# Kernel optimization log

Hardware: AMD Instinct MI355X
Metric: run time of the kernel (lower is better)

Reference implementation:

```python
import jax, jax.numpy as jnp
import numpy as np

N_EMBED = 768
NUM_HEADS = 12
HEAD_SIZE = N_EMBED // NUM_HEADS
EPS = 1e-6


def layer_norm(x, gamma, beta):
    # torch .var() is unbiased (ddof=1)
    mean = x.mean(-1, keepdims=True)
    var = jnp.var(x, axis=-1, keepdims=True, ddof=1)
    xhat = (x - mean) / jnp.sqrt(var + EPS)
    return gamma * xhat + beta


def setup_inputs() -> dict:
    key = jax.random.key(0)
    ks = jax.random.split(key, 10)
    B, S, D = 4, 2048, N_EMBED
    H = 4 * D
    s = 0.02
    return {
        "x": jax.random.normal(ks[0], (B, S, D), jnp.float32),
        "wq": jax.random.normal(ks[1], (D, D), jnp.float32) * s,
        "wk": jax.random.normal(ks[2], (D, D), jnp.float32) * s,
        "wv": jax.random.normal(ks[3], (D, D), jnp.float32) * s,
        "wo": jax.random.normal(ks[4], (D, D), jnp.float32) * s,
        "w1": jax.random.normal(ks[5], (D, H), jnp.float32) * s,
        "b1": jnp.zeros((H,), jnp.float32),
        "w2": jax.random.normal(ks[6], (H, D), jnp.float32) * s,
        "b2": jnp.zeros((D,), jnp.float32),
        "gamma1": jnp.ones((D,), jnp.float32),
        "beta1": jnp.zeros((D,), jnp.float32),
        "gamma2": jnp.ones((D,), jnp.float32),
        "beta2": jnp.zeros((D,), jnp.float32),
    }


def reference(x, wq, wk, wv, wo, w1, b1, w2, b2, gamma1, beta1, gamma2, beta2):
    B, S, D = x.shape
    Hh, hs = NUM_HEADS, HEAD_SIZE

    # --- pre-LN causal self-attention ---
    xn = layer_norm(x, gamma1, beta1)
    q = (xn @ wq).reshape(B, S, Hh, hs).transpose(0, 2, 1, 3)  # [B,H,S,hs]
    k = (xn @ wk).reshape(B, S, Hh, hs).transpose(0, 2, 1, 3)
    v = (xn @ wv).reshape(B, S, Hh, hs).transpose(0, 2, 1, 3)

    scale = 1.0 / np.sqrt(hs).astype(np.float32)
    scores = jnp.einsum("bhqd,bhkd->bhqk", q, k) * scale  # [B,H,S,S]
    causal = jnp.tril(jnp.ones((S, S), bool))
    scores = jnp.where(causal, scores, -jnp.inf)
    weights = jax.nn.softmax(scores, axis=-1)
    attn = jnp.einsum("bhqk,bhkd->bhqd", weights, v)  # [B,H,S,hs]
    attn = attn.transpose(0, 2, 1, 3).reshape(B, S, D)
    x = x + attn @ wo

    # --- pre-LN MLP ---
    xn = layer_norm(x, gamma2, beta2)
    h = jax.nn.relu(xn @ w1 + b1)
    x = x + (h @ w2 + b2)
    return x
```

## Files before the change

### kernel.cpp

```cpp
#include <hip/hip_runtime.h>
#include <hip/hip_bf16.h>
#include <math.h>

#define BATCH 4
#define SEQ   2048
#define DMODEL 768
#define NHEAD 12
#define HS    64
#define HID   3072
#define NROWS (BATCH*SEQ)
#define QKVN  (3*DMODEL)
#define EPS   1e-6f

typedef __attribute__((ext_vector_type(8))) short bf16x8;
typedef __attribute__((ext_vector_type(4))) float f32x4;

__device__ inline ushort f2b(float f) {
    union { float f; unsigned u; } x; x.f = f;
    unsigned u = x.u;
    unsigned r = (u + 0x7FFFu + ((u >> 16) & 1u)) >> 16;
    return (ushort)r;
}

#define GLDS16(g, l) __builtin_amdgcn_global_load_lds( \
    (const __attribute__((address_space(1))) void*)(g), \
    (__attribute__((address_space(3))) void*)(l), 16, 0, 0)

__global__ __launch_bounds__(256) void convert_w4(const float* __restrict__ p0,
                                                  const float* __restrict__ p1,
                                                  const float* __restrict__ p2,
                                                  const float* __restrict__ p3,
                                                  ushort* __restrict__ out) {
    const float* srcs[4] = { p0, p1, p2, p3 };
    const float* in = srcs[blockIdx.z];
    ushort* dst = out + (size_t)blockIdx.z * DMODEL * DMODEL;
    __shared__ float tile[32][33];
    const int bx = blockIdx.x * 32;
    const int by = blockIdx.y * 32;
    const int tx = threadIdx.x & 31, ty = threadIdx.x >> 5;
    #pragma unroll
    for (int i = 0; i < 32; i += 8)
        tile[ty + i][tx] = in[(size_t)(by + ty + i) * DMODEL + bx + tx];
    __syncthreads();
    #pragma unroll
    for (int i = 0; i < 32; i += 8)
        dst[(size_t)(bx + ty + i) * DMODEL + by + tx] = f2b(tile[tx][ty + i]);
}

__global__ __launch_bounds__(256) void convert_w(const float* __restrict__ in,
                                                 ushort* __restrict__ out,
                                                 int K, int N) {
    __shared__ float tile[32][33];
    const int bx = blockIdx.x * 32;
    const int by = blockIdx.y * 32;
    const int tx = threadIdx.x & 31, ty = threadIdx.x >> 5;
    #pragma unroll
    for (int i = 0; i < 32; i += 8)
        tile[ty + i][tx] = in[(size_t)(by + ty + i) * N + bx + tx];
    __syncthreads();
    #pragma unroll
    for (int i = 0; i < 32; i += 8)
        out[(size_t)(bx + ty + i) * K + by + tx] = f2b(tile[tx][ty + i]);
}

__global__ __launch_bounds__(256) void transpose_v(const ushort* __restrict__ v,
                                                   ushort* __restrict__ vt) {
    const int st = blockIdx.x;
    const int bh = blockIdx.y;
    const int b = bh / NHEAD, h = bh % NHEAD;
    const ushort* src = v + ((size_t)b * SEQ) * QKVN + h * HS;
    ushort* dst = vt + ((size_t)bh * HS) * SEQ;
    __shared__ ushort t[64][65];
    const int col = threadIdx.x & 63;
    const int r0  = (threadIdx.x >> 6) * 16;
    #pragma unroll
    for (int i = 0; i < 16; ++i)
        t[col][r0 + i] = src[(size_t)(st * 64 + r0 + i) * QKVN + col];
    __syncthreads();
    #pragma unroll
    for (int i = 0; i < 16; ++i)
        dst[(size_t)(r0 + i) * SEQ + st * 64 + col] = t[r0 + i][col];
}

__global__ __launch_bounds__(256) void ln_kernel(const float* __restrict__ x,
                                                 const float* __restrict__ gamma,
                                                 const float* __restrict__ beta,
                                                 ushort* __restrict__ out) {
    const int row = blockIdx.x;
    const float* xr = x + (size_t)row * DMODEL;
    float s = 0.f, s2 = 0.f;
    for (int i = threadIdx.x; i < DMODEL; i += 256) {
        float v = xr[i];
        s += v; s2 += v * v;
    }
    for (int off = 32; off > 0; off >>= 1) {
        s  += __shfl_down(s,  off, 64);
        s2 += __shfl_down(s2, off, 64);
    }
    __shared__ float shs[4], shs2[4];
    int wid = threadIdx.x >> 6, lane = threadIdx.x & 63;
    if (lane == 0) { shs[wid] = s; shs2[wid] = s2; }
    __syncthreads();
    __shared__ float smean, srstd;
    if (threadIdx.x == 0) {
        float S  = shs[0] + shs[1] + shs[2] + shs[3];
        float S2 = shs2[0] + shs2[1] + shs2[2] + shs2[3];
        float mean = S / DMODEL;
        float var  = (S2 - DMODEL * mean * mean) / (DMODEL - 1);
        smean = mean;
        srstd = rsqrtf(var + EPS);
    }
    __syncthreads();
    float mean = smean, rstd = srstd;
    ushort* orow = out + (size_t)row * DMODEL;
    for (int i = threadIdx.x; i < DMODEL; i += 256) {
        orow[i] = f2b(gamma[i] * (xr[i] - mean) * rstd + beta[i]);
    }
}

#define GN 128
#define GK 64
template<int MI>
__global__ __launch_bounds__(256, 4) void gemm_mfma(const ushort* __restrict__ A,
                                                    const ushort* __restrict__ Bt,
                                                    const float* __restrict__ bias,
                                                    const float* __restrict__ res,
                                                    float* __restrict__ C,
                                                    ushort* __restrict__ Cb,
                                                    int M, int N, int K, int do_relu,
                                                    int scale_q) {
    constexpr int GM = MI * 32;
    __shared__ ushort As[GM * GK];
    __shared__ ushort Bs[GN * GK];
    const int tid  = threadIdx.x;
    const int lane = tid & 63, wave = tid >> 6;
    const int l16  = lane & 15, quad = lane >> 4;
    const int wr = wave >> 1, wc = wave & 1;
    const int row0 = blockIdx.y * GM, col0 = blockIdx.x * GN;

    f32x4 acc[MI][4];
    #pragma unroll
    for (int i = 0; i < MI; ++i)
        #pragma unroll
        for (int j = 0; j < 4; ++j) acc[i][j] = (f32x4){0.f, 0.f, 0.f, 0.f};

    const ushort* Asrc[MI];
    const ushort* Bsrc[4];
    #pragma unroll
    for (int i = 0; i < MI; ++i) {
        int c = tid + i * 256, m = c >> 3, j = c & 7;
        Asrc[i] = A + (size_t)(row0 + m) * K + (j ^ (m & 7)) * 8;
    }
    #pragma unroll
    for (int i = 0; i < 4; ++i) {
        int c = tid + i * 256, m = c >> 3, j = c & 7;
        Bsrc[i] = Bt + (size_t)(col0 + m) * K + (j ^ (m & 7)) * 8;
    }

    for (int k0 = 0; k0 < K; k0 += GK) {
        #pragma unroll
        for (int i = 0; i < MI; ++i) GLDS16(Asrc[i] + k0, As + (tid + i * 256) * 8);
        #pragma unroll
        for (int i = 0; i < 4; ++i)  GLDS16(Bsrc[i] + k0, Bs + (tid + i * 256) * 8);
        __syncthreads();

        #pragma unroll
        for (int s = 0; s < 2; ++s) {
            bf16x8 af[MI], bfr[4];
            #pragma unroll
            for (int i = 0; i < MI; ++i) {
                int m = wr * (MI * 16) + i * 16 + l16;
                af[i] = *(const bf16x8*)&As[(m * 8 + (((s << 2) | quad) ^ (m & 7))) * 8];
            }
            #pragma unroll
            for (int j = 0; j < 4; ++j) {
                int n = wc * 64 + j * 16 + l16;
                bfr[j] = *(const bf16x8*)&Bs[(n * 8 + (((s << 2) | quad) ^ (n & 7))) * 8];
            }
            #pragma unroll
            for (int i = 0; i < MI; ++i)
                #pragma unroll
                for (int j = 0; j < 4; ++j)
                    acc[i][j] = __builtin_amdgcn_mfma_f32_16x16x32_bf16(af[i], bfr[j], acc[i][j], 0, 0, 0);
        }
        __syncthreads();
    }

    #pragma unroll
    for (int i = 0; i < MI; ++i) {
        #pragma unroll
        for (int r = 0; r < 4; ++r) {
            int row = row0 + wr * (MI * 16) + i * 16 + quad * 4 + r;
            #pragma unroll
            for (int j = 0; j < 4; ++j) {
                int col = col0 + wc * 64 + j * 16 + l16;
                float v = acc[i][j][r];
                if (bias) v += bias[col];
                if (do_relu) v = fmaxf(v, 0.f);
                if (scale_q && col < DMODEL) v *= 0.125f;
                if (res) v += res[(size_t)row * N + col];
                if (Cb) Cb[(size_t)row * N + col] = f2b(v);
                else    C [(size_t)row * N + col] = v;
            }
        }
    }
}

#define TQ 64
#define TK 64
#define PPAD 72
#define NQT (SEQ / TQ)

__global__ __launch_bounds__(256, 3) void fattn_kernel(const ushort* __restrict__ q,
                                                       const ushort* __restrict__ k,
                                                       const ushort* __restrict__ vt,
                                                       ushort* __restrict__ o,
                                                       int ldqkv) {
    const int pair = blockIdx.x;
    const int qts[2] = { pair, NQT - 1 - pair };
    const int bh = blockIdx.y;
    const int b = bh / NHEAD, h = bh % NHEAD;
    const int tid  = threadIdx.x;
    const int wave = tid >> 6;
    const int lane = tid & 63;
    const int l16  = lane & 15;
    const int quad = lane >> 4;

    __shared__ ushort Ks[2][TK * 64];
    __shared__ ushort Vs[2][HS * 64];
    __shared__ ushort Ps[4][16][PPAD];

    const size_t base  = ((size_t)b * SEQ) * ldqkv + (size_t)h * HS;
    const size_t baseO = ((size_t)b * SEQ) * DMODEL + (size_t)h * HS;
    const ushort* vth = vt + ((size_t)bh * HS) * SEQ;

    const int r0 = tid >> 3, j0 = (tid & 7) ^ (r0 & 7);
    const int r1 = (tid + 256) >> 3, j1 = (tid & 7) ^ (r1 & 7);
    const ushort* Ksrc0 = k + base + (size_t)r0 * ldqkv + j0 * 8;
    const ushort* Ksrc1 = k + base + (size_t)r1 * ldqkv + j1 * 8;
    const ushort* Vsrc0 = vth + (size_t)r0 * SEQ + j0 * 8;
    const ushort* Vsrc1 = vth + (size_t)r1 * SEQ + j1 * 8;

    bf16x8 qf[2][2];
    #pragma unroll
    for (int t = 0; t < 2; ++t) {
        int qrow = qts[t] * TQ + wave * 16 + l16;
        const ushort* qp = q + base + (size_t)qrow * ldqkv + quad * 8;
        qf[t][0] = *(const bf16x8*)(qp);
        qf[t][1] = *(const bf16x8*)(qp + 32);
    }

    f32x4 Oacc[2][4];
    float lrow[2][4];
    #pragma unroll
    for (int t = 0; t < 2; ++t) {
        #pragma unroll
        for (int f = 0; f < 4; ++f) Oacc[t][f] = (f32x4){0.f, 0.f, 0.f, 0.f};
        #pragma unroll
        for (int r = 0; r < 4; ++r) lrow[t][r] = 0.f;
    }

    const int ktiles = qts[1] + 1;
    GLDS16(Ksrc0, &Ks[0][tid * 8]);
    GLDS16(Ksrc1, &Ks[0][(tid + 256) * 8]);
    GLDS16(Vsrc0, &Vs[0][tid * 8]);
    GLDS16(Vsrc1, &Vs[0][(tid + 256) * 8]);

    for (int kt = 0; kt < ktiles; ++kt) {
        const int p = kt & 1;
        __syncthreads();
        if (kt + 1 < ktiles) {
            const size_t ko = (size_t)(kt + 1) * TK;
            GLDS16(Ksrc0 + ko * ldqkv, &Ks[p ^ 1][tid * 8]);
            GLDS16(Ksrc1 + ko * ldqkv, &Ks[p ^ 1][(tid + 256) * 8]);
            GLDS16(Vsrc0 + ko,         &Vs[p ^ 1][tid * 8]);
            GLDS16(Vsrc1 + ko,         &Vs[p ^ 1][(tid + 256) * 8]);
        }

        bf16x8 kb[4][2], vb[4][2];
        #pragma unroll
        for (int f = 0; f < 4; ++f) {
            int row = f * 16 + l16;
            kb[f][0] = *(const bf16x8*)&Ks[p][(row * 8 + (quad ^ (row & 7))) * 8];
            kb[f][1] = *(const bf16x8*)&Ks[p][(row * 8 + ((4 | quad) ^ (row & 7))) * 8];
            vb[f][0] = *(const bf16x8*)&Vs[p][(row * 8 + (quad ^ (row & 7))) * 8];
            vb[f][1] = *(const bf16x8*)&Vs[p][(row * 8 + ((4 | quad) ^ (row & 7))) * 8];
        }

        #pragma unroll
        for (int t = 0; t < 2; ++t) {
            const int qt = qts[t];
            if (kt > qt) continue;

            f32x4 S[4];
            #pragma unroll
            for (int f = 0; f < 4; ++f) {
                f32x4 a = (f32x4){0.f, 0.f, 0.f, 0.f};
                a = __builtin_amdgcn_mfma_f32_16x16x32_bf16(qf[t][0], kb[f][0], a, 0, 0, 0);
                a = __builtin_amdgcn_mfma_f32_16x16x32_bf16(qf[t][1], kb[f][1], a, 0, 0, 0);
                S[f] = a;
            }

            const int qrow_base = qt * TQ + wave * 16 + quad * 4;
            if (kt == qt) {
                #pragma unroll
                for (int f = 0; f < 4; ++f) {
                    int key = kt * TK + f * 16 + l16;
                    #pragma unroll
                    for (int r = 0; r < 4; ++r)
                        if (key > qrow_base + r) S[f][r] = -INFINITY;
                }
            }

            #pragma unroll
            for (int f = 0; f < 4; ++f) {
                #pragma unroll
                for (int r = 0; r < 4; ++r) {
                    float pv = __expf(S[f][r]);
                    S[f][r] = pv;
                    lrow[t][r] += pv;
                }
            }

            #pragma unroll
            for (int f = 0; f < 4; ++f)
                #pragma unroll
                for (int r = 0; r < 4; ++r)
                    Ps[wave][quad * 4 + r][f * 16 + l16] = f2b(S[f][r]);

            bf16x8 pa0 = *(const bf16x8*)&Ps[wave][l16][quad * 8];
            bf16x8 pa1 = *(const bf16x8*)&Ps[wave][l16][32 + quad * 8];
            #pragma unroll
            for (int f = 0; f < 4; ++f) {
                Oacc[t][f] = __builtin_amdgcn_mfma_f32_16x16x32_bf16(pa0, vb[f][0], Oacc[t][f], 0, 0, 0);
                Oacc[t][f] = __builtin_amdgcn_mfma_f32_16x16x32_bf16(pa1, vb[f][1], Oacc[t][f], 0, 0, 0);
            }
        }
    }

    #pragma unroll
    for (int t = 0; t < 2; ++t) {
        const int qrow = qts[t] * TQ + wave * 16 + quad * 4;
        #pragma unroll
        for (int r = 0; r < 4; ++r) {
            float l = lrow[t][r];
            #pragma unroll
            for (int m = 1; m < 16; m <<= 1) l += __shfl_xor(l, m, 64);
            float invl = 1.f / l;
            #pragma unroll
            for (int f = 0; f < 4; ++f)
                o[baseO + (size_t)(qrow + r) * DMODEL + f * 16 + l16] = f2b(Oacc[t][f][r] * invl);
        }
    }
}

extern "C" void kernel_launch(void* const* d_in, const int* in_sizes, int n_in,
                              void* d_out, int out_size, void* d_ws, size_t ws_size,
                              hipStream_t stream) {
    const float* x      = (const float*)d_in[0];
    const float* wq     = (const float*)d_in[1];
    const float* wk     = (const float*)d_in[2];
    const float* wv     = (const float*)d_in[3];
    const float* wo     = (const float*)d_in[4];
    const float* w1     = (const float*)d_in[5];
    const float* b1     = (const float*)d_in[6];
    const float* w2     = (const float*)d_in[7];
    const float* b2     = (const float*)d_in[8];
    const float* gamma1 = (const float*)d_in[9];
    const float* beta1  = (const float*)d_in[10];
    const float* gamma2 = (const float*)d_in[11];
    const float* beta2  = (const float*)d_in[12];
    float* out = (float*)d_out;

    char* ws = (char*)d_ws;
    ushort* buf_xn   = (ushort*)ws;
    ushort* buf_attn = buf_xn;
    ushort* buf_qkv  = (ushort*)(ws + 12582912);
    ushort* buf_h    = buf_qkv;
    ushort* w_qkv    = (ushort*)(ws + 12582912 + 50331648);
    ushort* w_ot     = w_qkv + (size_t)QKVN * DMODEL;
    ushort* w_1t     = w_ot + (size_t)DMODEL * DMODEL;
    ushort* w_2t     = w_1t + (size_t)HID * DMODEL;
    ushort* buf_vt   = (ushort*)d_out;

    convert_w4<<<dim3(DMODEL/32, DMODEL/32, 4), 256, 0, stream>>>(wq, wk, wv, wo, w_qkv);
    convert_w<<<dim3(HID/32,    DMODEL/32), 256, 0, stream>>>(w1, w_1t, DMODEL, HID);
    convert_w<<<dim3(DMODEL/32, HID/32),    256, 0, stream>>>(w2, w_2t, HID, DMODEL);

    ln_kernel<<<NROWS, 256, 0, stream>>>(x, gamma1, beta1, buf_xn);
    gemm_mfma<4><<<dim3(QKVN/GN, NROWS/128), 256, 0, stream>>>(buf_xn, w_qkv, nullptr, nullptr,
                                                               nullptr, buf_qkv, NROWS, QKVN, DMODEL, 0, 1);
    transpose_v<<<dim3(SEQ/64, BATCH*NHEAD), 256, 0, stream>>>(buf_qkv + 2*DMODEL, buf_vt);
    fattn_kernel<<<dim3(NQT/2, BATCH*NHEAD), 256, 0, stream>>>(buf_qkv, buf_qkv + DMODEL,
                                                               buf_vt, buf_attn, QKVN);
    gemm_mfma<2><<<dim3(DMODEL/GN, NROWS/64), 256, 0, stream>>>(buf_attn, w_ot, nullptr, x,
                                                                out, nullptr, NROWS, DMODEL, DMODEL, 0, 0);
    ln_kernel<<<NROWS, 256, 0, stream>>>(out, gamma2, beta2, buf_xn);
    gemm_mfma<4><<<dim3(HID/GN, NROWS/128), 256, 0, stream>>>(buf_xn, w_1t, b1, nullptr,
                                                              nullptr, buf_h, NROWS, HID, DMODEL, 1, 0);
    gemm_mfma<2><<<dim3(DMODEL/GN, NROWS/64), 256, 0, stream>>>(buf_h, w_2t, b2, out,
                                                                out, nullptr, NROWS, DMODEL, HID, 0, 0);
}
```

Measured before the change: 417.5 us.

## Double-buffer GEMM LDS tiles and remap workgroup IDs across XCDs

Result: slower. 431.1 us (+3.2%).

```diff
diff --git a/kernel.cpp b/kernel.cpp
--- a/kernel.cpp
+++ b/kernel.cpp
@@ -121,7 +121,7 @@
 #define GN 128
 #define GK 64
 template<int MI>
-__global__ __launch_bounds__(256, 4) void gemm_mfma(const ushort* __restrict__ A,
+__global__ __launch_bounds__(256, 3) void gemm_mfma(const ushort* __restrict__ A,
                                                     const ushort* __restrict__ Bt,
                                                     const float* __restrict__ bias,
                                                     const float* __restrict__ res,
@@ -130,13 +130,22 @@
                                                     int M, int N, int K, int do_relu,
                                                     int scale_q) {
     constexpr int GM = MI * 32;
-    __shared__ ushort As[GM * GK];
-    __shared__ ushort Bs[GN * GK];
+    __shared__ ushort As[2][GM * GK];
+    __shared__ ushort Bs[2][GN * GK];
     const int tid  = threadIdx.x;
     const int lane = tid & 63, wave = tid >> 6;
     const int l16  = lane & 15, quad = lane >> 4;
     const int wr = wave >> 1, wc = wave & 1;
-    const int row0 = blockIdx.y * GM, col0 = blockIdx.x * GN;
+
+    const int nwg = gridDim.x * gridDim.y;
+    int id = blockIdx.y * gridDim.x + blockIdx.x;
+    if ((nwg & 7) == 0) {
+        const int chunk = nwg >> 3;
+        id = (id & 7) * chunk + (id >> 3);
+    }
+    const int bx = id % gridDim.x;
+    const int by = id / gridDim.x;
+    const int row0 = by * GM, col0 = bx * GN;
 
     f32x4 acc[MI][4];
     #pragma unroll
@@ -157,12 +166,22 @@
         Bsrc[i] = Bt + (size_t)(col0 + m) * K + (j ^ (m & 7)) * 8;
     }
 
-    for (int k0 = 0; k0 < K; k0 += GK) {
-        #pragma unroll
-        for (int i = 0; i < MI; ++i) GLDS16(Asrc[i] + k0, As + (tid + i * 256) * 8);
-        #pragma unroll
-        for (int i = 0; i < 4; ++i)  GLDS16(Bsrc[i] + k0, Bs + (tid + i * 256) * 8);
+    const int nk = K / GK;
+    #pragma unroll
+    for (int i = 0; i < MI; ++i) GLDS16(Asrc[i], &As[0][(tid + i * 256) * 8]);
+    #pragma unroll
+    for (int i = 0; i < 4; ++i)  GLDS16(Bsrc[i], &Bs[0][(tid + i * 256) * 8]);
+
+    for (int kt = 0; kt < nk; ++kt) {
+        const int p = kt & 1;
         __syncthreads();
+        if (kt + 1 < nk) {
+            const int k1 = (kt + 1) * GK;
+            #pragma unroll
+            for (int i = 0; i < MI; ++i) GLDS16(Asrc[i] + k1, &As[p ^ 1][(tid + i * 256) * 8]);
+            #pragma unroll
+            for (int i = 0; i < 4; ++i)  GLDS16(Bsrc[i] + k1, &Bs[p ^ 1][(tid + i * 256) * 8]);
+        }
 
         #pragma unroll
         for (int s = 0; s < 2; ++s) {
@@ -170,12 +189,12 @@
             #pragma unroll
             for (int i = 0; i < MI; ++i) {
                 int m = wr * (MI * 16) + i * 16 + l16;
-                af[i] = *(const bf16x8*)&As[(m * 8 + (((s << 2) | quad) ^ (m & 7))) * 8];
+                af[i] = *(const bf16x8*)&As[p][(m * 8 + (((s << 2) | quad) ^ (m & 7))) * 8];
             }
             #pragma unroll
             for (int j = 0; j < 4; ++j) {
                 int n = wc * 64 + j * 16 + l16;
-                bfr[j] = *(const bf16x8*)&Bs[(n * 8 + (((s << 2) | quad) ^ (n & 7))) * 8];
+                bfr[j] = *(const bf16x8*)&Bs[p][(n * 8 + (((s << 2) | quad) ^ (n & 7))) * 8];
             }
             #pragma unroll
             for (int i = 0; i < MI; ++i)
@@ -183,7 +202,6 @@
                 for (int j = 0; j < 4; ++j)
                     acc[i][j] = __builtin_amdgcn_mfma_f32_16x16x32_bf16(af[i], bfr[j], acc[i][j], 0, 0, 0);
         }
-        __syncthreads();
     }
 
     #pragma unroll
```
